# Performance work log

Measured on AMD Instinct MI355X. Metric: run time of the kernel, lower is better.

## Reference

```python
import jax, jax.numpy as jnp
import numpy as np

V, L, D, DEMO, HID, N = 20000, 128, 256, 70, 1024, 2048


def setup_inputs() -> dict:
    key = jax.random.key(0)
    ks = jax.random.split(key, 16)
    s = 1.0 / np.sqrt(D)
    inp = {
        # learned parameters
        "E": jax.random.normal(ks[0], (V, D), jnp.float32) * 0.02,
        "Wq": jax.random.normal(ks[1], (D, D), jnp.float32) * s,
        "Wk": jax.random.normal(ks[2], (D, D), jnp.float32) * s,
        "Wv": jax.random.normal(ks[3], (D, D), jnp.float32) * s,
        "c_attn": jnp.ones((1,), jnp.float32) * 0.1,   # time_weight_net coefficient (attention decay)
        "c_pool": jnp.ones((1,), jnp.float32) * 0.5,   # history_repr Q_base-style pooling decay
        "W1": jax.random.normal(ks[4], (D + DEMO, HID), jnp.float32) * (1.0 / np.sqrt(D + DEMO)),
        "b1": jnp.zeros((HID,), jnp.float32),
        "W2": jax.random.normal(ks[5], (HID, 1), jnp.float32) * (1.0 / np.sqrt(HID)),
        "b2": jnp.zeros((1,), jnp.float32),
        # batched ragged task instances
        "demo": jax.random.normal(ks[6], (N, DEMO), jnp.float32),
        "hist_times": jax.random.uniform(ks[7], (N, L), jnp.float32) * 10.0,
        "event_time": jax.random.uniform(ks[8], (N,), jnp.float32) * 10.0 + 10.0,
        "labels": jax.random.randint(ks[9], (N,), 0, 2).astype(jnp.float32),
        "codes": jax.random.randint(ks[10], (N, L), 0, V),
        "lengths": jax.random.randint(ks[11], (N,), 1, L + 1).astype(jnp.int32),
    }
    return inp


def reference(E, Wq, Wk, Wv, c_attn, c_pool, W1, b1, W2, b2,
              demo, hist_times, event_time, labels, codes, lengths):
    POS_WEIGHT = 2.0
    NEG = jnp.float32(-1e9)
    mask = jnp.arange(L)[None, :] < lengths[:, None]            # [N, L] valid history positions

    emb = E[codes]                                              # [N, L, D] gather
    q = jnp.einsum('nld,de->nle', emb, Wq)
    k = jnp.einsum('nld,de->nle', emb, Wk)
    v = jnp.einsum('nld,de->nle', emb, Wv)

    # time-aware self-attention over each ragged history (masked)
    scores = jnp.einsum('nid,njd->nij', q, k) / jnp.sqrt(jnp.float32(D))
    dt = jnp.abs(hist_times[:, :, None] - hist_times[:, None, :])  # [N, L, L]
    scores = scores - c_attn[0] * dt
    scores = jnp.where(mask[:, None, :], scores, NEG)
    attn = jax.nn.softmax(scores, axis=-1)
    events = jnp.einsum('nij,njd->nid', attn, v)                # [N, L, D]

    # history_repr: time-decayed pooling toward event_time
    w = -c_pool[0] * (event_time[:, None] - hist_times)         # [N, L]
    w = jnp.where(mask, w, NEG)
    w = jax.nn.softmax(w, axis=-1)
    repr_ = jnp.einsum('nl,nld->nd', w, events)                 # [N, D]

    # disease/death classifier: demographics + history repr -> logit
    x = jnp.concatenate([demo, repr_], axis=-1)                 # [N, DEMO+D]
    h = jax.nn.relu(x @ W1 + b1)
    logit = (h @ W2 + b2)[:, 0]                                 # [N]

    # BCEWithLogitsLoss with pos_weight, averaged over valid predictions
    loss = -(POS_WEIGHT * labels * jax.nn.log_sigmoid(logit)
             + (1.0 - labels) * jax.nn.log_sigmoid(-logit))
    avg_loss = jnp.mean(loss)

    reg_loss = jnp.sum(c_attn ** 2) + jnp.sum(c_pool ** 2)      # time_weight_net.get_reg_loss()
    return avg_loss + reg_loss
```

## Files before the change

### kernel.cpp

```cpp
#include <hip/hip_runtime.h>
#include <hip/hip_bf16.h>
#include <math.h>
#include <stdint.h>

#define VV 20000
#define LL 128
#define DD 256
#define DEMO_ 70
#define HID_ 1024
#define NN 2048

typedef __attribute__((ext_vector_type(8))) short short8;
typedef __attribute__((ext_vector_type(4))) float f32x4;

__device__ __forceinline__ float bf2f(uint32_t u) {
    union { uint32_t u; float f; } c; c.u = u << 16; return c.f;
}
__device__ __forceinline__ uint32_t f2bf(float f) {
    union { float f; uint32_t u; } c; c.f = f;
    return (c.u + 0x7fffu + ((c.u >> 16) & 1u)) >> 16;
}

__device__ __forceinline__ int sw_off(int row, int col) {
    return (row << 8) + ((((col >> 3) ^ (row & 7)) << 3) | (col & 7));
}

__global__ __launch_bounds__(256) void k_pre(
    const float* __restrict__ Wq, const float* __restrict__ Wk,
    const float* __restrict__ Wv, const float* __restrict__ W1,
    const float* __restrict__ ca, const float* __restrict__ cp,
    const int* __restrict__ lens,
    unsigned short* __restrict__ Mxf, unsigned short* __restrict__ W1f,
    int* __restrict__ order, float* __restrict__ z, float* __restrict__ out)
{
    __shared__ float sm[DD];
    __shared__ int cnt[9], off[9], cur[9];
    const int b = blockIdx.x, t = threadIdx.x;

    if (b < 256) {
        int e = b;
        sm[t] = Wq[(size_t)e * DD + t];
        __syncthreads();
        const float4* wk4 = (const float4*)(Wk + (size_t)t * DD);
        const float4* wq4 = (const float4*)sm;
        float4 acc = make_float4(0.f, 0.f, 0.f, 0.f);
        for (int c = 0; c < DD / 4; ++c) {
            float4 a = wq4[c]; float4 bb = wk4[c];
            acc.x += a.x * bb.x; acc.y += a.y * bb.y;
            acc.z += a.z * bb.z; acc.w += a.w * bb.w;
        }
        float val = acc.x + acc.y + acc.z + acc.w;
        int frag = (e >> 4) * 8 + (t >> 5);
        int pos  = (((t >> 3) & 3) * 16 + (e & 15)) * 8 + (t & 7);
        Mxf[(size_t)frag * 512 + pos] = (unsigned short)f2bf(val);
    } else if (b < 256 + 1408) {
        int idx = b - 256;
        int k = idx % 352, by = idx / 352;
        int h = t + 256 * by;
        float val;
        if (k >= 326) {
            val = 0.f;
        } else if (k < DEMO_) {
            val = W1[(size_t)k * HID_ + h];
        } else {
            int e = k - DEMO_;
            sm[t] = Wv[(size_t)e * DD + t];
            __syncthreads();
            float acc = 0.f;
            for (int n = 0; n < DD; ++n)
                acc += sm[n] * W1[(size_t)(DEMO_ + n) * HID_ + h];
            val = acc;
        }
        int frag = (h >> 4) * 11 + (k >> 5);
        int pos  = (((k >> 3) & 3) * 16 + (h & 15)) * 8 + (k & 7);
        W1f[(size_t)frag * 512 + pos] = (unsigned short)f2bf(val);
    } else if (b == 1664) {
        if (t < 9) cnt[t] = 0;
        __syncthreads();
        for (int i = t; i < NN; i += 256)
            atomicAdd(&cnt[(lens[i] + 15) >> 4], 1);
        __syncthreads();
        if (t == 0) {
            int acc = 0;
            for (int k = 8; k >= 1; --k) { off[k] = acc; acc += cnt[k]; cur[k] = off[k]; }
        }
        __syncthreads();
        for (int i = t; i < NN; i += 256) {
            int key = (lens[i] + 15) >> 4;
            int pos = atomicAdd(&cur[key], 1);
            order[pos] = i;
        }
    } else {
        for (int i = t; i < NN; i += 256) z[i] = 0.f;
        if (t == 0) out[0] = ca[0] * ca[0] + cp[0] * cp[0];
    }
}

__global__ __launch_bounds__(512, 4) void k_main(
    const float* __restrict__ E,
    const float* __restrict__ ht,  const float* __restrict__ evt_t,
    const int* __restrict__ codes, const int* __restrict__ lens,
    const float* __restrict__ ca_p, const float* __restrict__ cp_p,
    const unsigned short* __restrict__ Mxf,
    const int* __restrict__ order,
    unsigned short* __restrict__ Rbf)
{
    __shared__ __align__(16) unsigned short emb_u[LL * DD];
    __shared__ float times_s[LL];
    __shared__ int   codes_s[LL];
    __shared__ float w_s[LL];
    __shared__ float apart[8][LL];
    __shared__ float rp_part[8][DD];
    __shared__ float asum[LL];

    const int n = order[blockIdx.x];
    const int tid = threadIdx.x, wv = tid >> 6, ln = tid & 63;
    const int q = ln >> 4, m = ln & 15;
    const int len = lens[n];
    const int it_n = (len + 15) >> 4;
    const float ca = ca_p[0], cp = cp_p[0];
    const float evt = evt_t[n];

    short8 bB[2][8];
    #pragma unroll
    for (int nt = 0; nt < 2; ++nt)
        #pragma unroll
        for (int kk = 0; kk < 8; ++kk)
            bB[nt][kk] = *(const short8*)(Mxf + (size_t)((wv * 2 + nt) * 8 + kk) * 512 + ln * 8);

    if (tid < LL) {
        bool v = tid < len;
        times_s[tid] = v ? ht[(size_t)n * LL + tid] : 0.f;
        codes_s[tid] = v ? codes[(size_t)n * LL + tid] : 0;
    }
    if (wv == 0) {
        float t0 = (ln      < len) ? ht[(size_t)n * LL + ln]      : 0.f;
        float t1 = (ln + 64 < len) ? ht[(size_t)n * LL + ln + 64] : 0.f;
        float e0 = (ln      < len) ? __expf(cp * (t0 - evt)) : 0.f;
        float e1 = (ln + 64 < len) ? __expf(cp * (t1 - evt)) : 0.f;
        float smm = e0 + e1;
        for (int o = 32; o; o >>= 1) smm += __shfl_xor(smm, o, 64);
        float inv = 1.f / smm;
        if (ln      < len) w_s[ln]      = e0 * inv;
        if (ln + 64 < len) w_s[ln + 64] = e1 * inv;
    }
    __syncthreads();

    for (int l0 = wv; l0 < len; l0 += 32) {
        float4 v[4];
        #pragma unroll
        for (int u = 0; u < 4; ++u) {
            int l = l0 + u * 8;
            if (l < len)
                v[u] = ((const float4*)(E + (size_t)codes_s[l] * DD))[ln];
        }
        #pragma unroll
        for (int u = 0; u < 4; ++u) {
            int l = l0 + u * 8;
            if (l < len)
                *(uint2*)&emb_u[sw_off(l, 4 * ln)] =
                    make_uint2(f2bf(v[u].x) | (f2bf(v[u].y) << 16),
                               f2bf(v[u].z) | (f2bf(v[u].w) << 16));
        }
    }
    __syncthreads();

    short8 aC[8];
    for (int it = 0; it < it_n; ++it) {
        f32x4 h0 = (f32x4)0.f, h1 = (f32x4)0.f;
        #pragma unroll
        for (int kk = 0; kk < 8; ++kk) {
            short8 af = *(const short8*)&emb_u[sw_off(it * 16 + m, kk * 32 + q * 8)];
            if (it == wv) aC[kk] = af;
            h0 = __builtin_amdgcn_mfma_f32_16x16x32_bf16(af, bB[0][kk], h0, 0, 0, 0);
            h1 = __builtin_amdgcn_mfma_f32_16x16x32_bf16(af, bB[1][kk], h1, 0, 0, 0);
        }
        __syncthreads();
        #pragma unroll
        for (int r = 0; r < 4; ++r) {
            int row = it * 16 + q * 4 + r;
            emb_u[sw_off(row, wv * 32 + m)]      = (unsigned short)f2bf(h0[r]);
            emb_u[sw_off(row, wv * 32 + 16 + m)] = (unsigned short)f2bf(h1[r]);
        }
    }
    __syncthreads();

    if (wv < it_n) {
        f32x4 sac[8];
        #pragma unroll
        for (int jt = 0; jt < 8; ++jt) sac[jt] = (f32x4)0.f;
        for (int jt = 0; jt < it_n; ++jt) {
            #pragma unroll
            for (int kk = 0; kk < 8; ++kk) {
                short8 bH = *(const short8*)&emb_u[sw_off(jt * 16 + m, kk * 32 + q * 8)];
                sac[jt] = __builtin_amdgcn_mfma_f32_16x16x32_bf16(aC[kk], bH, sac[jt], 0, 0, 0);
            }
        }
        int i_base = wv * 16 + q * 4;
        float ti[4]; bool vR[4]; float rowsum[4];
        #pragma unroll
        for (int r = 0; r < 4; ++r) {
            vR[r] = (i_base + r) < len;
            ti[r] = times_s[i_base + r];
            rowsum[r] = 0.f;
        }
        for (int jt = 0; jt < it_n; ++jt) {
            int jcol = jt * 16 + m;
            bool vC = jcol < len;
            float tj = times_s[jcol];
            #pragma unroll
            for (int r = 0; r < 4; ++r) {
                float arg = sac[jt][r] * 0.0625f - ca * fabsf(ti[r] - tj);
                float p = (vR[r] && vC) ? __expf(arg) : 0.f;
                sac[jt][r] = p;
                rowsum[r] += p;
            }
        }
        #pragma unroll
        for (int r = 0; r < 4; ++r) {
            float s = rowsum[r];
            s += __shfl_xor(s, 1, 64); s += __shfl_xor(s, 2, 64);
            s += __shfl_xor(s, 4, 64); s += __shfl_xor(s, 8, 64);
            rowsum[r] = s;
        }
        float sc[4];
        #pragma unroll
        for (int r = 0; r < 4; ++r)
            sc[r] = (vR[r] && rowsum[r] > 0.f) ? w_s[i_base + r] / rowsum[r] : 0.f;
        for (int jt = 0; jt < it_n; ++jt) {
            float v = sc[0] * sac[jt][0] + sc[1] * sac[jt][1]
                    + sc[2] * sac[jt][2] + sc[3] * sac[jt][3];
            v += __shfl_xor(v, 16, 64);
            v += __shfl_xor(v, 32, 64);
            if (q == 0) apart[wv][jt * 16 + m] = v;
        }
    }
    __syncthreads();

    if (tid < LL) {
        float s = 0.f;
        for (int r = 0; r < it_n; ++r) s += apart[r][tid];
        asum[tid] = s;
    }
    __syncthreads();

    if (wv < it_n) {
        float aw = asum[wv * 16 + m];
        #pragma unroll
        for (int kk = 0; kk < 8; ++kk) {
            float v[8];
            #pragma unroll
            for (int j = 0; j < 8; ++j)
                v[j] = aw * bf2f((uint32_t)(unsigned short)aC[kk][j]);
            #pragma unroll
            for (int o = 1; o <= 8; o <<= 1)
                #pragma unroll
                for (int j = 0; j < 8; ++j)
                    v[j] += __shfl_xor(v[j], o, 64);
            if (m < 8)
                rp_part[wv][kk * 32 + q * 8 + m] = v[m];
        }
    }
    __syncthreads();
    if (tid < DD) {
        float r = 0.f;
        for (int t = 0; t < it_n; ++t) r += rp_part[t][tid];
        Rbf[(size_t)n * DD + tid] = (unsigned short)f2bf(r);
    }
}

__global__ __launch_bounds__(256) void k_mlp(
    const float* __restrict__ demo,
    const float* __restrict__ b1,   const float* __restrict__ W2,
    const unsigned short* __restrict__ Rbf,
    const unsigned short* __restrict__ W1f,
    float* __restrict__ z)
{
    __shared__ __align__(16) unsigned short xs[16][360];
    __shared__ float W2s[256];
    __shared__ float b1s[256];
    __shared__ float wred[4][16];

    const int tid = threadIdx.x, wv = tid >> 6, ln = tid & 63;
    const int q = ln >> 4, m = ln & 15;
    const int s0 = blockIdx.x * 16;
    const int by = blockIdx.y;
    const int hbase = by * 256;

    W2s[tid] = W2[hbase + tid];
    b1s[tid] = b1[hbase + tid];
    for (int s = 0; s < 16; ++s) {
        if (tid < DEMO_) xs[s][tid] = (unsigned short)f2bf(demo[(size_t)(s0 + s) * DEMO_ + tid]);
        xs[s][DEMO_ + tid] = Rbf[(size_t)(s0 + s) * DD + tid];
        if (tid < 34) xs[s][326 + tid] = 0;
    }
    __syncthreads();

    f32x4 cacc[4];
    #pragma unroll
    for (int ntl = 0; ntl < 4; ++ntl) cacc[ntl] = (f32x4)0.f;

    for (int kk = 0; kk < 11; ++kk) {
        short8 af = *(const short8*)&xs[m][kk * 32 + q * 8];
        #pragma unroll
        for (int ntl = 0; ntl < 4; ++ntl) {
            int frag = (by * 16 + wv * 4 + ntl) * 11 + kk;
            short8 bfd = *(const short8*)(W1f + (size_t)frag * 512 + ln * 8);
            cacc[ntl] = __builtin_amdgcn_mfma_f32_16x16x32_bf16(af, bfd, cacc[ntl], 0, 0, 0);
        }
    }

    float ls0 = 0.f, ls1 = 0.f, ls2 = 0.f, ls3 = 0.f;
    #pragma unroll
    for (int ntl = 0; ntl < 4; ++ntl) {
        int hl = wv * 64 + ntl * 16 + m;
        float bb = b1s[hl], w2v = W2s[hl];
        ls0 += fmaxf(cacc[ntl][0] + bb, 0.f) * w2v;
        ls1 += fmaxf(cacc[ntl][1] + bb, 0.f) * w2v;
        ls2 += fmaxf(cacc[ntl][2] + bb, 0.f) * w2v;
        ls3 += fmaxf(cacc[ntl][3] + bb, 0.f) * w2v;
    }
    #pragma unroll
    for (int o = 1; o <= 8; o <<= 1) {
        ls0 += __shfl_xor(ls0, o, 64); ls1 += __shfl_xor(ls1, o, 64);
        ls2 += __shfl_xor(ls2, o, 64); ls3 += __shfl_xor(ls3, o, 64);
    }
    if (m == 0) {
        wred[wv][q * 4 + 0] = ls0; wred[wv][q * 4 + 1] = ls1;
        wred[wv][q * 4 + 2] = ls2; wred[wv][q * 4 + 3] = ls3;
    }
    __syncthreads();
    if (tid < 16)
        atomicAdd(&z[s0 + tid], wred[0][tid] + wred[1][tid] + wred[2][tid] + wred[3][tid]);
}

__global__ __launch_bounds__(256) void k_loss(const float* __restrict__ labels,
                                              const float* __restrict__ b2,
                                              const float* __restrict__ z,
                                              float* __restrict__ out) {
    __shared__ float red[4];
    int tid = threadIdx.x, wv = tid >> 6;
    int i = blockIdx.x * 256 + tid;
    float zz = z[i] + b2[0];
    float y = labels[i];
    float lg = log1pf(__expf(-fabsf(zz)));
    float loss = 2.f * y * (fmaxf(-zz, 0.f) + lg) + (1.f - y) * (fmaxf(zz, 0.f) + lg);
    for (int o = 32; o; o >>= 1) loss += __shfl_xor(loss, o, 64);
    if ((tid & 63) == 0) red[wv] = loss;
    __syncthreads();
    if (tid == 0)
        atomicAdd(out, (red[0] + red[1] + red[2] + red[3]) * (1.f / (float)NN));
}

extern "C" void kernel_launch(void* const* d_in, const int* in_sizes, int n_in,
                              void* d_out, int out_size, void* d_ws, size_t ws_size,
                              hipStream_t stream) {
    const float* E      = (const float*)d_in[0];
    const float* Wq     = (const float*)d_in[1];
    const float* Wk     = (const float*)d_in[2];
    const float* Wv     = (const float*)d_in[3];
    const float* ca     = (const float*)d_in[4];
    const float* cp     = (const float*)d_in[5];
    const float* W1     = (const float*)d_in[6];
    const float* b1     = (const float*)d_in[7];
    const float* W2     = (const float*)d_in[8];
    const float* b2     = (const float*)d_in[9];
    const float* demo   = (const float*)d_in[10];
    const float* ht     = (const float*)d_in[11];
    const float* evt    = (const float*)d_in[12];
    const float* labels = (const float*)d_in[13];
    const int*   codes  = (const int*)d_in[14];
    const int*   lens   = (const int*)d_in[15];
    float* out = (float*)d_out;

    unsigned short* Mxf = (unsigned short*)d_ws;
    unsigned short* W1f = (unsigned short*)((char*)d_ws + 131072);
    unsigned short* Rbf = (unsigned short*)((char*)d_ws + 851968);
    float*          zar = (float*)((char*)d_ws + 1900544);
    int*            ord = (int*)((char*)d_ws + 1908736);

    hipLaunchKernelGGL(k_pre,  dim3(1666), dim3(256), 0, stream,
                       Wq, Wk, Wv, W1, ca, cp, lens, Mxf, W1f, ord, zar, out);
    hipLaunchKernelGGL(k_main, dim3(NN), dim3(512), 0, stream,
                       E, ht, evt, codes, lens, ca, cp, Mxf, ord, Rbf);
    hipLaunchKernelGGL(k_mlp,  dim3(NN / 16, 4), dim3(256), 0, stream,
                       demo, b1, W2, Rbf, W1f, zar);
    hipLaunchKernelGGL(k_loss, dim3(NN / 256), dim3(256), 0, stream, labels, b2, zar, out);
}
```

Measured before the change: 227.8 us.

## Persist k_main blocks over four samples, register-tile Wv·W1 fold, widen MLP tiles

k_main now launches 512 persistent blocks that each process four samples from the length-sorted order, so the Mxf B fragments are loaded into registers once per block instead of once per sample. The waves-per-EU attribute is pinned to 4. In k_pre, the Wv·W1 fold is register-tiled so each block computes 8 rows by 2 columns per thread, which replaces 1408 one-row blocks and cuts redundant W1 reads. k_mlp processes 32 samples per block so each W1f fragment load feeds two MFMAs. The risk is load imbalance, since blocks with stride-512 sample assignment may get uneven total lengths, and fewer blocks means less parallelism to hide latency.

```diff
diff --git a/kernel.cpp b/kernel.cpp
--- a/kernel.cpp
+++ b/kernel.cpp
@@ -34,6 +34,7 @@
     int* __restrict__ order, float* __restrict__ z, float* __restrict__ out)
 {
     __shared__ float sm[DD];
+    __shared__ float wvs[8][DD];
     __shared__ int cnt[9], off[9], cur[9];
     const int b = blockIdx.x, t = threadIdx.x;
 
@@ -53,28 +54,47 @@
         int frag = (e >> 4) * 8 + (t >> 5);
         int pos  = (((t >> 3) & 3) * 16 + (e & 15)) * 8 + (t & 7);
         Mxf[(size_t)frag * 512 + pos] = (unsigned short)f2bf(val);
-    } else if (b < 256 + 1408) {
-        int idx = b - 256;
-        int k = idx % 352, by = idx / 352;
-        int h = t + 256 * by;
-        float val;
-        if (k >= 326) {
-            val = 0.f;
-        } else if (k < DEMO_) {
-            val = W1[(size_t)k * HID_ + h];
-        } else {
-            int e = k - DEMO_;
-            sm[t] = Wv[(size_t)e * DD + t];
-            __syncthreads();
-            float acc = 0.f;
-            for (int n = 0; n < DD; ++n)
-                acc += sm[n] * W1[(size_t)(DEMO_ + n) * HID_ + h];
-            val = acc;
-        }
-        int frag = (h >> 4) * 11 + (k >> 5);
-        int pos  = (((k >> 3) & 3) * 16 + (h & 15)) * 8 + (k & 7);
-        W1f[(size_t)frag * 512 + pos] = (unsigned short)f2bf(val);
-    } else if (b == 1664) {
+    } else if (b < 320) {
+        int f = b - 256, kg = f >> 1, hh = f & 1;
+        #pragma unroll
+        for (int r = 0; r < 8; ++r)
+            wvs[r][t] = Wv[(size_t)(kg * 8 + r) * DD + t];
+        __syncthreads();
+        int h0 = hh * 512 + t;
+        float acc[8][2];
+        #pragma unroll
+        for (int r = 0; r < 8; ++r) { acc[r][0] = 0.f; acc[r][1] = 0.f; }
+        #pragma unroll 2
+        for (int n = 0; n < DD; ++n) {
+            float a = W1[(size_t)(DEMO_ + n) * HID_ + h0];
+            float c = W1[(size_t)(DEMO_ + n) * HID_ + h0 + 256];
+            #pragma unroll
+            for (int r = 0; r < 8; ++r) {
+                float w = wvs[r][n];
+                acc[r][0] += w * a; acc[r][1] += w * c;
+            }
+        }
+        #pragma unroll
+        for (int r = 0; r < 8; ++r)
+            #pragma unroll
+            for (int e2 = 0; e2 < 2; ++e2) {
+                int k = DEMO_ + kg * 8 + r;
+                int h = h0 + e2 * 256;
+                int frag = (h >> 4) * 11 + (k >> 5);
+                int pos  = (((k >> 3) & 3) * 16 + (h & 15)) * 8 + (k & 7);
+                W1f[(size_t)frag * 512 + pos] = (unsigned short)f2bf(acc[r][e2]);
+            }
+    } else if (b < 352) {
+        int g = b - 320;
+        for (int idx = g * 256 + t; idx < 96 * 1024; idx += 32 * 256) {
+            int kk = idx >> 10, h = idx & 1023;
+            int k = kk < DEMO_ ? kk : kk + 256;
+            float val = kk < DEMO_ ? W1[(size_t)kk * HID_ + h] : 0.f;
+            int frag = (h >> 4) * 11 + (k >> 5);
+            int pos  = (((k >> 3) & 3) * 16 + (h & 15)) * 8 + (k & 7);
+            W1f[(size_t)frag * 512 + pos] = (unsigned short)f2bf(val);
+        }
+    } else if (b == 352) {
         if (t < 9) cnt[t] = 0;
         __syncthreads();
         for (int i = t; i < NN; i += 256)
@@ -96,7 +116,8 @@
     }
 }
 
-__global__ __launch_bounds__(512, 4) void k_main(
+__global__ __launch_bounds__(512, 4) __attribute__((amdgpu_waves_per_eu(4, 4)))
+void k_main(
     const float* __restrict__ E,
     const float* __restrict__ ht,  const float* __restrict__ evt_t,
     const int* __restrict__ codes, const int* __restrict__ lens,
@@ -113,13 +134,9 @@
     __shared__ float rp_part[8][DD];
     __shared__ float asum[LL];
 
-    const int n = order[blockIdx.x];
     const int tid = threadIdx.x, wv = tid >> 6, ln = tid & 63;
     const int q = ln >> 4, m = ln & 15;
-    const int len = lens[n];
-    const int it_n = (len + 15) >> 4;
     const float ca = ca_p[0], cp = cp_p[0];
-    const float evt = evt_t[n];
 
     short8 bB[2][8];
     #pragma unroll
@@ -128,144 +145,152 @@
         for (int kk = 0; kk < 8; ++kk)
             bB[nt][kk] = *(const short8*)(Mxf + (size_t)((wv * 2 + nt) * 8 + kk) * 512 + ln * 8);
 
-    if (tid < LL) {
-        bool v = tid < len;
-        times_s[tid] = v ? ht[(size_t)n * LL + tid] : 0.f;
-        codes_s[tid] = v ? codes[(size_t)n * LL + tid] : 0;
-    }
-    if (wv == 0) {
-        float t0 = (ln      < len) ? ht[(size_t)n * LL + ln]      : 0.f;
-        float t1 = (ln + 64 < len) ? ht[(size_t)n * LL + ln + 64] : 0.f;
-        float e0 = (ln      < len) ? __expf(cp * (t0 - evt)) : 0.f;
-        float e1 = (ln + 64 < len) ? __expf(cp * (t1 - evt)) : 0.f;
-        float smm = e0 + e1;
-        for (int o = 32; o; o >>= 1) smm += __shfl_xor(smm, o, 64);
-        float inv = 1.f / smm;
-        if (ln      < len) w_s[ln]      = e0 * inv;
-        if (ln + 64 < len) w_s[ln + 64] = e1 * inv;
-    }
-    __syncthreads();
-
-    for (int l0 = wv; l0 < len; l0 += 32) {
-        float4 v[4];
-        #pragma unroll
-        for (int u = 0; u < 4; ++u) {
-            int l = l0 + u * 8;
-            if (l < len)
-                v[u] = ((const float4*)(E + (size_t)codes_s[l] * DD))[ln];
-        }
-        #pragma unroll
-        for (int u = 0; u < 4; ++u) {
-            int l = l0 + u * 8;
-            if (l < len)
-                *(uint2*)&emb_u[sw_off(l, 4 * ln)] =
-                    make_uint2(f2bf(v[u].x) | (f2bf(v[u].y) << 16),
-                               f2bf(v[u].z) | (f2bf(v[u].w) << 16));
-        }
-    }
-    __syncthreads();
-
-    short8 aC[8];
-    for (int it = 0; it < it_n; ++it) {
-        f32x4 h0 = (f32x4)0.f, h1 = (f32x4)0.f;
-        #pragma unroll
-        for (int kk = 0; kk < 8; ++kk) {
-            short8 af = *(const short8*)&emb_u[sw_off(it * 16 + m, kk * 32 + q * 8)];
-            if (it == wv) aC[kk] = af;
-            h0 = __builtin_amdgcn_mfma_f32_16x16x32_bf16(af, bB[0][kk], h0, 0, 0, 0);
-            h1 = __builtin_amdgcn_mfma_f32_16x16x32_bf16(af, bB[1][kk], h1, 0, 0, 0);
-        }
-        __syncthreads();
-        #pragma unroll
-        for (int r = 0; r < 4; ++r) {
-            int row = it * 16 + q * 4 + r;
-            emb_u[sw_off(row, wv * 32 + m)]      = (unsigned short)f2bf(h0[r]);
-            emb_u[sw_off(row, wv * 32 + 16 + m)] = (unsigned short)f2bf(h1[r]);
-        }
-    }
-    __syncthreads();
-
-    if (wv < it_n) {
-        f32x4 sac[8];
-        #pragma unroll
-        for (int jt = 0; jt < 8; ++jt) sac[jt] = (f32x4)0.f;
-        for (int jt = 0; jt < it_n; ++jt) {
+    for (int rep = 0; rep < 4; ++rep) {
+        const int n = order[blockIdx.x + 512 * rep];
+        const int len = lens[n];
+        const int it_n = (len + 15) >> 4;
+        const float evt = evt_t[n];
+
+        if (tid < LL) {
+            bool v = tid < len;
+            times_s[tid] = v ? ht[(size_t)n * LL + tid] : 0.f;
+            codes_s[tid] = v ? codes[(size_t)n * LL + tid] : 0;
+        }
+        if (wv == 0) {
+            float t0 = (ln      < len) ? ht[(size_t)n * LL + ln]      : 0.f;
+            float t1 = (ln + 64 < len) ? ht[(size_t)n * LL + ln + 64] : 0.f;
+            float e0 = (ln      < len) ? __expf(cp * (t0 - evt)) : 0.f;
+            float e1 = (ln + 64 < len) ? __expf(cp * (t1 - evt)) : 0.f;
+            float smm = e0 + e1;
+            for (int o = 32; o; o >>= 1) smm += __shfl_xor(smm, o, 64);
+            float inv = 1.f / smm;
+            if (ln      < len) w_s[ln]      = e0 * inv;
+            if (ln + 64 < len) w_s[ln + 64] = e1 * inv;
+        }
+        __syncthreads();
+
+        for (int l0 = wv; l0 < len; l0 += 32) {
+            float4 v[4];
+            #pragma unroll
+            for (int u = 0; u < 4; ++u) {
+                int l = l0 + u * 8;
+                if (l < len)
+                    v[u] = ((const float4*)(E + (size_t)codes_s[l] * DD))[ln];
+            }
+            #pragma unroll
+            for (int u = 0; u < 4; ++u) {
+                int l = l0 + u * 8;
+                if (l < len)
+                    *(uint2*)&emb_u[sw_off(l, 4 * ln)] =
+                        make_uint2(f2bf(v[u].x) | (f2bf(v[u].y) << 16),
+                                   f2bf(v[u].z) | (f2bf(v[u].w) << 16));
+            }
+        }
+        __syncthreads();
+
+        short8 aC[8];
+        for (int it = 0; it < it_n; ++it) {
+            f32x4 h0 = (f32x4)0.f, h1 = (f32x4)0.f;
             #pragma unroll
             for (int kk = 0; kk < 8; ++kk) {
-                short8 bH = *(const short8*)&emb_u[sw_off(jt * 16 + m, kk * 32 + q * 8)];
-                sac[jt] = __builtin_amdgcn_mfma_f32_16x16x32_bf16(aC[kk], bH, sac[jt], 0, 0, 0);
-            }
-        }
-        int i_base = wv * 16 + q * 4;
-        float ti[4]; bool vR[4]; float rowsum[4];
-        #pragma unroll
-        for (int r = 0; r < 4; ++r) {
-            vR[r] = (i_base + r) < len;
-            ti[r] = times_s[i_base + r];
-            rowsum[r] = 0.f;
-        }
-        for (int jt = 0; jt < it_n; ++jt) {
-            int jcol = jt * 16 + m;
-            bool vC = jcol < len;
-            float tj = times_s[jcol];
+                short8 af = *(const short8*)&emb_u[sw_off(it * 16 + m, kk * 32 + q * 8)];
+                if (it == wv) aC[kk] = af;
+                h0 = __builtin_amdgcn_mfma_f32_16x16x32_bf16(af, bB[0][kk], h0, 0, 0, 0);
+                h1 = __builtin_amdgcn_mfma_f32_16x16x32_bf16(af, bB[1][kk], h1, 0, 0, 0);
+            }
+            __syncthreads();
             #pragma unroll
             for (int r = 0; r < 4; ++r) {
-                float arg = sac[jt][r] * 0.0625f - ca * fabsf(ti[r] - tj);
-                float p = (vR[r] && vC) ? __expf(arg) : 0.f;
-                sac[jt][r] = p;
-                rowsum[r] += p;
-            }
-        }
-        #pragma unroll
-        for (int r = 0; r < 4; ++r) {
-            float s = rowsum[r];
-            s += __shfl_xor(s, 1, 64); s += __shfl_xor(s, 2, 64);
-            s += __shfl_xor(s, 4, 64); s += __shfl_xor(s, 8, 64);
-            rowsum[r] = s;
-        }
-        float sc[4];
-        #pragma unroll
-        for (int r = 0; r < 4; ++r)
-            sc[r] = (vR[r] && rowsum[r] > 0.f) ? w_s[i_base + r] / rowsum[r] : 0.f;
-        for (int jt = 0; jt < it_n; ++jt) {
-            float v = sc[0] * sac[jt][0] + sc[1] * sac[jt][1]
-                    + sc[2] * sac[jt][2] + sc[3] * sac[jt][3];
-            v += __shfl_xor(v, 16, 64);
-            v += __shfl_xor(v, 32, 64);
-            if (q == 0) apart[wv][jt * 16 + m] = v;
-        }
-    }
-    __syncthreads();
-
-    if (tid < LL) {
-        float s = 0.f;
-        for (int r = 0; r < it_n; ++r) s += apart[r][tid];
-        asum[tid] = s;
-    }
-    __syncthreads();
-
-    if (wv < it_n) {
-        float aw = asum[wv * 16 + m];
-        #pragma unroll
-        for (int kk = 0; kk < 8; ++kk) {
-            float v[8];
-            #pragma unroll
-            for (int j = 0; j < 8; ++j)
-                v[j] = aw * bf2f((uint32_t)(unsigned short)aC[kk][j]);
-            #pragma unroll
-            for (int o = 1; o <= 8; o <<= 1)
+                int row = it * 16 + q * 4 + r;
+                emb_u[sw_off(row, wv * 32 + m)]      = (unsigned short)f2bf(h0[r]);
+                emb_u[sw_off(row, wv * 32 + 16 + m)] = (unsigned short)f2bf(h1[r]);
+            }
+        }
+        __syncthreads();
+
+        if (wv < it_n) {
+            f32x4 sac[8];
+            #pragma unroll
+            for (int jt = 0; jt < 8; ++jt) sac[jt] = (f32x4)0.f;
+            for (int jt = 0; jt < it_n; ++jt) {
+                #pragma unroll
+                for (int kk = 0; kk < 8; ++kk) {
+                    short8 bH = *(const short8*)&emb_u[sw_off(jt * 16 + m, kk * 32 + q * 8)];
+                    sac[jt] = __builtin_amdgcn_mfma_f32_16x16x32_bf16(aC[kk], bH, sac[jt], 0, 0, 0);
+                }
+            }
+            int i_base = wv * 16 + q * 4;
+            float ti[4]; bool vR[4]; float rowsum[4];
+            #pragma unroll
+            for (int r = 0; r < 4; ++r) {
+                vR[r] = (i_base + r) < len;
+                ti[r] = times_s[i_base + r];
+                rowsum[r] = 0.f;
+            }
+            for (int jt = 0; jt < it_n; ++jt) {
+                int jcol = jt * 16 + m;
+                bool vC = jcol < len;
+                float tj = times_s[jcol];
+                #pragma unroll
+                for (int r = 0; r < 4; ++r) {
+                    float arg = sac[jt][r] * 0.0625f - ca * fabsf(ti[r] - tj);
+                    float p = (vR[r] && vC) ? __expf(arg) : 0.f;
+                    sac[jt][r] = p;
+                    rowsum[r] += p;
+                }
+            }
+            #pragma unroll
+            for (int r = 0; r < 4; ++r) {
+                float s = rowsum[r];
+                s += __shfl_xor(s, 1, 64); s += __shfl_xor(s, 2, 64);
+                s += __shfl_xor(s, 4, 64); s += __shfl_xor(s, 8, 64);
+                rowsum[r] = s;
+            }
+            float sc[4];
+            #pragma unroll
+            for (int r = 0; r < 4; ++r)
+                sc[r] = (vR[r] && rowsum[r] > 0.f) ? w_s[i_base + r] / rowsum[r] : 0.f;
+            for (int jt = 0; jt < it_n; ++jt) {
+                float v = sc[0] * sac[jt][0] + sc[1] * sac[jt][1]
+                        + sc[2] * sac[jt][2] + sc[3] * sac[jt][3];
+                v += __shfl_xor(v, 16, 64);
+                v += __shfl_xor(v, 32, 64);
+                if (q == 0) apart[wv][jt * 16 + m] = v;
+            }
+        }
+        __syncthreads();
+
+        if (tid < LL) {
+            float s = 0.f;
+            for (int r = 0; r < it_n; ++r) s += apart[r][tid];
+            asum[tid] = s;
+        }
+        __syncthreads();
+
+        if (wv < it_n) {
+            float aw = asum[wv * 16 + m];
+            #pragma unroll
+            for (int kk = 0; kk < 8; ++kk) {
+                float v[8];
                 #pragma unroll
                 for (int j = 0; j < 8; ++j)
-                    v[j] += __shfl_xor(v[j], o, 64);
-            if (m < 8)
-                rp_part[wv][kk * 32 + q * 8 + m] = v[m];
-        }
-    }
-    __syncthreads();
-    if (tid < DD) {
-        float r = 0.f;
-        for (int t = 0; t < it_n; ++t) r += rp_part[t][tid];
-        Rbf[(size_t)n * DD + tid] = (unsigned short)f2bf(r);
+                    v[j] = aw * bf2f((uint32_t)(unsigned short)aC[kk][j]);
+                #pragma unroll
+                for (int o = 1; o <= 8; o <<= 1)
+                    #pragma unroll
+                    for (int j = 0; j < 8; ++j)
+                        v[j] += __shfl_xor(v[j], o, 64);
+                if (m < 8)
+                    rp_part[wv][kk * 32 + q * 8 + m] = v[m];
+            }
+        }
+        __syncthreads();
+        if (tid < DD) {
+            float r = 0.f;
+            for (int t2 = 0; t2 < it_n; ++t2) r += rp_part[t2][tid];
+            Rbf[(size_t)n * DD + tid] = (unsigned short)f2bf(r);
+        }
+        __syncthreads();
     }
 }
 
@@ -276,61 +301,68 @@
     const unsigned short* __restrict__ W1f,
     float* __restrict__ z)
 {
-    __shared__ __align__(16) unsigned short xs[16][360];
+    __shared__ __align__(16) unsigned short xs[32][360];
     __shared__ float W2s[256];
     __shared__ float b1s[256];
-    __shared__ float wred[4][16];
+    __shared__ float wred[4][32];
 
     const int tid = threadIdx.x, wv = tid >> 6, ln = tid & 63;
     const int q = ln >> 4, m = ln & 15;
-    const int s0 = blockIdx.x * 16;
+    const int s0 = blockIdx.x * 32;
     const int by = blockIdx.y;
     const int hbase = by * 256;
 
     W2s[tid] = W2[hbase + tid];
     b1s[tid] = b1[hbase + tid];
-    for (int s = 0; s < 16; ++s) {
+    for (int s = 0; s < 32; ++s) {
         if (tid < DEMO_) xs[s][tid] = (unsigned short)f2bf(demo[(size_t)(s0 + s) * DEMO_ + tid]);
         xs[s][DEMO_ + tid] = Rbf[(size_t)(s0 + s) * DD + tid];
         if (tid < 34) xs[s][326 + tid] = 0;
     }
     __syncthreads();
 
-    f32x4 cacc[4];
+    f32x4 cacc[2][4];
     #pragma unroll
-    for (int ntl = 0; ntl < 4; ++ntl) cacc[ntl] = (f32x4)0.f;
+    for (int mt = 0; mt < 2; ++mt)
+        #pragma unroll
+        for (int ntl = 0; ntl < 4; ++ntl) cacc[mt][ntl] = (f32x4)0.f;
 
     for (int kk = 0; kk < 11; ++kk) {
-        short8 af = *(const short8*)&xs[m][kk * 32 + q * 8];
+        short8 af0 = *(const short8*)&xs[m][kk * 32 + q * 8];
+        short8 af1 = *(const short8*)&xs[16 + m][kk * 32 + q * 8];
         #pragma unroll
         for (int ntl = 0; ntl < 4; ++ntl) {
             int frag = (by * 16 + wv * 4 + ntl) * 11 + kk;
             short8 bfd = *(const short8*)(W1f + (size_t)frag * 512 + ln * 8);
-            cacc[ntl] = __builtin_amdgcn_mfma_f32_16x16x32_bf16(af, bfd, cacc[ntl], 0, 0, 0);
+            cacc[0][ntl] = __builtin_amdgcn_mfma_f32_16x16x32_bf16(af0, bfd, cacc[0][ntl], 0, 0, 0);
+            cacc[1][ntl] = __builtin_amdgcn_mfma_f32_16x16x32_bf16(af1, bfd, cacc[1][ntl], 0, 0, 0);
         }
     }
 
-    float ls0 = 0.f, ls1 = 0.f, ls2 = 0.f, ls3 = 0.f;
     #pragma unroll
-    for (int ntl = 0; ntl < 4; ++ntl) {
-        int hl = wv * 64 + ntl * 16 + m;
-        float bb = b1s[hl], w2v = W2s[hl];
-        ls0 += fmaxf(cacc[ntl][0] + bb, 0.f) * w2v;
-        ls1 += fmaxf(cacc[ntl][1] + bb, 0.f) * w2v;
-        ls2 += fmaxf(cacc[ntl][2] + bb, 0.f) * w2v;
-        ls3 += fmaxf(cacc[ntl][3] + bb, 0.f) * w2v;
-    }
-    #pragma unroll
-    for (int o = 1; o <= 8; o <<= 1) {
-        ls0 += __shfl_xor(ls0, o, 64); ls1 += __shfl_xor(ls1, o, 64);
-        ls2 += __shfl_xor(ls2, o, 64); ls3 += __shfl_xor(ls3, o, 64);
-    }
-    if (m == 0) {
-        wred[wv][q * 4 + 0] = ls0; wred[wv][q * 4 + 1] = ls1;
-        wred[wv][q * 4 + 2] = ls2; wred[wv][q * 4 + 3] = ls3;
+    for (int mt = 0; mt < 2; ++mt) {
+        float ls0 = 0.f, ls1 = 0.f, ls2 = 0.f, ls3 = 0.f;
+        #pragma unroll
+        for (int ntl = 0; ntl < 4; ++ntl) {
+            int hl = wv * 64 + ntl * 16 + m;
+            float bb = b1s[hl], w2v = W2s[hl];
+            ls0 += fmaxf(cacc[mt][ntl][0] + bb, 0.f) * w2v;
+            ls1 += fmaxf(cacc[mt][ntl][1] + bb, 0.f) * w2v;
+            ls2 += fmaxf(cacc[mt][ntl][2] + bb, 0.f) * w2v;
+            ls3 += fmaxf(cacc[mt][ntl][3] + bb, 0.f) * w2v;
+        }
+        #pragma unroll
+        for (int o = 1; o <= 8; o <<= 1) {
+            ls0 += __shfl_xor(ls0, o, 64); ls1 += __shfl_xor(ls1, o, 64);
+            ls2 += __shfl_xor(ls2, o, 64); ls3 += __shfl_xor(ls3, o, 64);
+        }
+        if (m == 0) {
+            wred[wv][mt * 16 + q * 4 + 0] = ls0; wred[wv][mt * 16 + q * 4 + 1] = ls1;
+            wred[wv][mt * 16 + q * 4 + 2] = ls2; wred[wv][mt * 16 + q * 4 + 3] = ls3;
+        }
     }
     __syncthreads();
-    if (tid < 16)
+    if (tid < 32)
         atomicAdd(&z[s0 + tid], wred[0][tid] + wred[1][tid] + wred[2][tid] + wred[3][tid]);
 }
 
@@ -379,11 +411,11 @@
     float*          zar = (float*)((char*)d_ws + 1900544);
     int*            ord = (int*)((char*)d_ws + 1908736);
 
-    hipLaunchKernelGGL(k_pre,  dim3(1666), dim3(256), 0, stream,
+    hipLaunchKernelGGL(k_pre,  dim3(354), dim3(256), 0, stream,
                        Wq, Wk, Wv, W1, ca, cp, lens, Mxf, W1f, ord, zar, out);
-    hipLaunchKernelGGL(k_main, dim3(NN), dim3(512), 0, stream,
+    hipLaunchKernelGGL(k_main, dim3(512), dim3(512), 0, stream,
                        E, ht, evt, codes, lens, ca, cp, Mxf, ord, Rbf);
-    hipLaunchKernelGGL(k_mlp,  dim3(NN / 16, 4), dim3(256), 0, stream,
+    hipLaunchKernelGGL(k_mlp,  dim3(NN / 32, 4), dim3(256), 0, stream,
                        demo, b1, W2, Rbf, W1f, zar);
     hipLaunchKernelGGL(k_loss, dim3(NN / 256), dim3(256), 0, stream, labels, b2, zar, out);
 }
```

Result: slower. 354.2 us (+55.5%).

## Fuse loss into MLP kernel, batch Wv·W1 precompute, shrink prep grid

Applied to the files above, without the earlier changes.

The MLP kernel now covers all 1024 hidden units per block instead of splitting over four y-blocks, so it can compute the BCE loss directly and the separate loss kernel, the z buffer and its zeroing are removed. The Wv·W1 fold in the prep kernel now has each block produce 8 output rows at once from a shared tile. This cuts redundant W1 reads and shrinks the grid from 1666 to 417 blocks. The trade is one fewer launch and less prep work against fewer, heavier MLP blocks (128 blocks, 16 accumulators per wave), which risks lower occupancy and parallelism.

```diff
diff --git a/kernel.cpp b/kernel.cpp
--- a/kernel.cpp
+++ b/kernel.cpp
@@ -31,9 +31,10 @@
     const float* __restrict__ ca, const float* __restrict__ cp,
     const int* __restrict__ lens,
     unsigned short* __restrict__ Mxf, unsigned short* __restrict__ W1f,
-    int* __restrict__ order, float* __restrict__ z, float* __restrict__ out)
+    int* __restrict__ order, float* __restrict__ out)
 {
     __shared__ float sm[DD];
+    __shared__ float wvs[8][DD];
     __shared__ int cnt[9], off[9], cur[9];
     const int b = blockIdx.x, t = threadIdx.x;
 
@@ -44,6 +45,7 @@
         const float4* wk4 = (const float4*)(Wk + (size_t)t * DD);
         const float4* wq4 = (const float4*)sm;
         float4 acc = make_float4(0.f, 0.f, 0.f, 0.f);
+        #pragma unroll 8
         for (int c = 0; c < DD / 4; ++c) {
             float4 a = wq4[c]; float4 bb = wk4[c];
             acc.x += a.x * bb.x; acc.y += a.y * bb.y;
@@ -53,28 +55,40 @@
         int frag = (e >> 4) * 8 + (t >> 5);
         int pos  = (((t >> 3) & 3) * 16 + (e & 15)) * 8 + (t & 7);
         Mxf[(size_t)frag * 512 + pos] = (unsigned short)f2bf(val);
-    } else if (b < 256 + 1408) {
-        int idx = b - 256;
-        int k = idx % 352, by = idx / 352;
-        int h = t + 256 * by;
-        float val;
-        if (k >= 326) {
-            val = 0.f;
-        } else if (k < DEMO_) {
-            val = W1[(size_t)k * HID_ + h];
-        } else {
-            int e = k - DEMO_;
-            sm[t] = Wv[(size_t)e * DD + t];
-            __syncthreads();
-            float acc = 0.f;
-            for (int n = 0; n < DD; ++n)
-                acc += sm[n] * W1[(size_t)(DEMO_ + n) * HID_ + h];
-            val = acc;
-        }
-        int frag = (h >> 4) * 11 + (k >> 5);
-        int pos  = (((k >> 3) & 3) * 16 + (h & 15)) * 8 + (k & 7);
-        W1f[(size_t)frag * 512 + pos] = (unsigned short)f2bf(val);
-    } else if (b == 1664) {
+    } else if (b < 384) {
+        int f = b - 256, kg = f >> 2, hh = f & 3;
+        #pragma unroll
+        for (int r = 0; r < 8; ++r)
+            wvs[r][t] = Wv[(size_t)(kg * 8 + r) * DD + t];
+        __syncthreads();
+        int h = hh * 256 + t;
+        float acc[8];
+        #pragma unroll
+        for (int r = 0; r < 8; ++r) acc[r] = 0.f;
+        #pragma unroll 4
+        for (int n = 0; n < DD; ++n) {
+            float a = W1[(size_t)(DEMO_ + n) * HID_ + h];
+            #pragma unroll
+            for (int r = 0; r < 8; ++r) acc[r] += wvs[r][n] * a;
+        }
+        #pragma unroll
+        for (int r = 0; r < 8; ++r) {
+            int k = DEMO_ + kg * 8 + r;
+            int frag = (h >> 4) * 11 + (k >> 5);
+            int pos  = (((k >> 3) & 3) * 16 + (h & 15)) * 8 + (k & 7);
+            W1f[(size_t)frag * 512 + pos] = (unsigned short)f2bf(acc[r]);
+        }
+    } else if (b < 416) {
+        int g = b - 384;
+        for (int idx = g * 256 + t; idx < 96 * 1024; idx += 32 * 256) {
+            int kk = idx >> 10, h = idx & 1023;
+            int k = kk < DEMO_ ? kk : kk + 256;
+            float val = kk < DEMO_ ? W1[(size_t)kk * HID_ + h] : 0.f;
+            int frag = (h >> 4) * 11 + (k >> 5);
+            int pos  = (((k >> 3) & 3) * 16 + (h & 15)) * 8 + (k & 7);
+            W1f[(size_t)frag * 512 + pos] = (unsigned short)f2bf(val);
+        }
+    } else {
         if (t < 9) cnt[t] = 0;
         __syncthreads();
         for (int i = t; i < NN; i += 256)
@@ -83,6 +97,7 @@
         if (t == 0) {
             int acc = 0;
             for (int k = 8; k >= 1; --k) { off[k] = acc; acc += cnt[k]; cur[k] = off[k]; }
+            out[0] = ca[0] * ca[0] + cp[0] * cp[0];
         }
         __syncthreads();
         for (int i = t; i < NN; i += 256) {
@@ -90,9 +105,6 @@
             int pos = atomicAdd(&cur[key], 1);
             order[pos] = i;
         }
-    } else {
-        for (int i = t; i < NN; i += 256) z[i] = 0.f;
-        if (t == 0) out[0] = ca[0] * ca[0] + cp[0] * cp[0];
     }
 }
 
@@ -264,31 +276,34 @@
     __syncthreads();
     if (tid < DD) {
         float r = 0.f;
-        for (int t = 0; t < it_n; ++t) r += rp_part[t][tid];
+        for (int t2 = 0; t2 < it_n; ++t2) r += rp_part[t2][tid];
         Rbf[(size_t)n * DD + tid] = (unsigned short)f2bf(r);
     }
 }
 
-__global__ __launch_bounds__(256) void k_mlp(
-    const float* __restrict__ demo,
+__global__ __launch_bounds__(256, 2) void k_mlp(
+    const float* __restrict__ demo, const float* __restrict__ labels,
     const float* __restrict__ b1,   const float* __restrict__ W2,
+    const float* __restrict__ b2,
     const unsigned short* __restrict__ Rbf,
     const unsigned short* __restrict__ W1f,
-    float* __restrict__ z)
+    float* __restrict__ out)
 {
     __shared__ __align__(16) unsigned short xs[16][360];
-    __shared__ float W2s[256];
-    __shared__ float b1s[256];
+    __shared__ float W2s[HID_];
+    __shared__ float b1s[HID_];
     __shared__ float wred[4][16];
+    __shared__ float lred[16];
 
     const int tid = threadIdx.x, wv = tid >> 6, ln = tid & 63;
     const int q = ln >> 4, m = ln & 15;
     const int s0 = blockIdx.x * 16;
-    const int by = blockIdx.y;
-    const int hbase = by * 256;
-
-    W2s[tid] = W2[hbase + tid];
-    b1s[tid] = b1[hbase + tid];
+
+    #pragma unroll
+    for (int hh = 0; hh < 4; ++hh) {
+        W2s[tid + 256 * hh] = W2[tid + 256 * hh];
+        b1s[tid + 256 * hh] = b1[tid + 256 * hh];
+    }
     for (int s = 0; s < 16; ++s) {
         if (tid < DEMO_) xs[s][tid] = (unsigned short)f2bf(demo[(size_t)(s0 + s) * DEMO_ + tid]);
         xs[s][DEMO_ + tid] = Rbf[(size_t)(s0 + s) * DD + tid];
@@ -296,15 +311,15 @@
     }
     __syncthreads();
 
-    f32x4 cacc[4];
-    #pragma unroll
-    for (int ntl = 0; ntl < 4; ++ntl) cacc[ntl] = (f32x4)0.f;
+    f32x4 cacc[16];
+    #pragma unroll
+    for (int ntl = 0; ntl < 16; ++ntl) cacc[ntl] = (f32x4)0.f;
 
     for (int kk = 0; kk < 11; ++kk) {
         short8 af = *(const short8*)&xs[m][kk * 32 + q * 8];
         #pragma unroll
-        for (int ntl = 0; ntl < 4; ++ntl) {
-            int frag = (by * 16 + wv * 4 + ntl) * 11 + kk;
+        for (int ntl = 0; ntl < 16; ++ntl) {
+            int frag = (wv * 16 + ntl) * 11 + kk;
             short8 bfd = *(const short8*)(W1f + (size_t)frag * 512 + ln * 8);
             cacc[ntl] = __builtin_amdgcn_mfma_f32_16x16x32_bf16(af, bfd, cacc[ntl], 0, 0, 0);
         }
@@ -312,8 +327,8 @@
 
     float ls0 = 0.f, ls1 = 0.f, ls2 = 0.f, ls3 = 0.f;
     #pragma unroll
-    for (int ntl = 0; ntl < 4; ++ntl) {
-        int hl = wv * 64 + ntl * 16 + m;
+    for (int ntl = 0; ntl < 16; ++ntl) {
+        int hl = wv * 256 + ntl * 16 + m;
         float bb = b1s[hl], w2v = W2s[hl];
         ls0 += fmaxf(cacc[ntl][0] + bb, 0.f) * w2v;
         ls1 += fmaxf(cacc[ntl][1] + bb, 0.f) * w2v;
@@ -330,26 +345,20 @@
         wred[wv][q * 4 + 2] = ls2; wred[wv][q * 4 + 3] = ls3;
     }
     __syncthreads();
-    if (tid < 16)
-        atomicAdd(&z[s0 + tid], wred[0][tid] + wred[1][tid] + wred[2][tid] + wred[3][tid]);
-}
-
-__global__ __launch_bounds__(256) void k_loss(const float* __restrict__ labels,
-                                              const float* __restrict__ b2,
-                                              const float* __restrict__ z,
-                                              float* __restrict__ out) {
-    __shared__ float red[4];
-    int tid = threadIdx.x, wv = tid >> 6;
-    int i = blockIdx.x * 256 + tid;
-    float zz = z[i] + b2[0];
-    float y = labels[i];
-    float lg = log1pf(__expf(-fabsf(zz)));
-    float loss = 2.f * y * (fmaxf(-zz, 0.f) + lg) + (1.f - y) * (fmaxf(zz, 0.f) + lg);
-    for (int o = 32; o; o >>= 1) loss += __shfl_xor(loss, o, 64);
-    if ((tid & 63) == 0) red[wv] = loss;
-    __syncthreads();
-    if (tid == 0)
-        atomicAdd(out, (red[0] + red[1] + red[2] + red[3]) * (1.f / (float)NN));
+    if (tid < 16) {
+        float z = wred[0][tid] + wred[1][tid] + wred[2][tid] + wred[3][tid] + b2[0];
+        float y = labels[s0 + tid];
+        float lg = log1pf(__expf(-fabsf(z)));
+        float loss = 2.f * y * (fmaxf(-z, 0.f) + lg) + (1.f - y) * (fmaxf(z, 0.f) + lg);
+        lred[tid] = loss;
+    }
+    __syncthreads();
+    if (tid == 0) {
+        float t = 0.f;
+        #pragma unroll
+        for (int i = 0; i < 16; ++i) t += lred[i];
+        atomicAdd(out, t * (1.f / (float)NN));
+    }
 }
 
 extern "C" void kernel_launch(void* const* d_in, const int* in_sizes, int n_in,
@@ -376,14 +385,12 @@
     unsigned short* Mxf = (unsigned short*)d_ws;
     unsigned short* W1f = (unsigned short*)((char*)d_ws + 131072);
     unsigned short* Rbf = (unsigned short*)((char*)d_ws + 851968);
-    float*          zar = (float*)((char*)d_ws + 1900544);
-    int*            ord = (int*)((char*)d_ws + 1908736);
-
-    hipLaunchKernelGGL(k_pre,  dim3(1666), dim3(256), 0, stream,
-                       Wq, Wk, Wv, W1, ca, cp, lens, Mxf, W1f, ord, zar, out);
+    int*            ord = (int*)((char*)d_ws + 1900544);
+
+    hipLaunchKernelGGL(k_pre,  dim3(417), dim3(256), 0, stream,
+                       Wq, Wk, Wv, W1, ca, cp, lens, Mxf, W1f, ord, out);
     hipLaunchKernelGGL(k_main, dim3(NN), dim3(512), 0, stream,
                        E, ht, evt, codes, lens, ca, cp, Mxf, ord, Rbf);
-    hipLaunchKernelGGL(k_mlp,  dim3(NN / 16, 4), dim3(256), 0, stream,
-                       demo, b1, W2, Rbf, W1f, zar);
-    hipLaunchKernelGGL(k_loss, dim3(NN / 256), dim3(256), 0, stream, labels, b2, zar, out);
-}
+    hipLaunchKernelGGL(k_mlp,  dim3(NN / 16), dim3(256), 0, stream,
+                       demo, labels, b1, W2, b2, Rbf, W1f, out);
+}
```

New measurement: 251.5 us. 1.1x slower.
